# Performance work log

Hardware: AMD Instinct MI355X
Metric: run time of the kernel (lower is better)

## Reference

```python
import jax, jax.numpy as jnp
import numpy as np
from jax import lax

BETA = 0.9   # membrane decay
THR = 1.0    # firing threshold (soft reset)
K = 10       # number of time bins
# spatial pyramid for original_shape=(100,368) under 4 stride-2 SAME convs
HW = [(50, 184), (25, 92), (13, 46), (7, 23)]
CH = [4, 8, 16, 32]


def conv(x, w, b, stride=1):
    y = lax.conv_general_dilated(x, w, (stride, stride), 'SAME',
                                 dimension_numbers=('NCHW', 'OIHW', 'NCHW'))
    return y + b[None, :, None, None]


def spike(u):
    # heaviside forward, sigmoid straight-through surrogate backward
    s = (u > 0.0).astype(u.dtype)
    sg = jax.nn.sigmoid(4.0 * u)
    return sg + lax.stop_gradient(s - sg)


def setup_inputs() -> dict:
    key = jax.random.key(0)
    ks = jax.random.split(key, 12)
    T, B = 1000, 1
    x = jax.random.normal(ks[0], (T, B, 1, 100, 368), jnp.float32)

    def w(k, o, i, kh=3, kw=3):
        return 0.1 * jax.random.normal(k, (o, i, kh, kw), jnp.float32)

    inp = {'x': x}
    cin = [1] + CH[:3]
    for li in range(4):
        inp['w%d' % (li + 1)] = w(ks[1 + li], CH[li], cin[li])
        inp['b%d' % (li + 1)] = jnp.zeros((CH[li],), jnp.float32)
    sc = [2 * K * c for c in CH]  # skip channels: [80,160,320,640]
    inp['dw4'] = w(ks[5], 64, sc[3]); inp['db4'] = jnp.zeros((64,), jnp.float32)
    inp['dw3'] = w(ks[6], 32, 64 + sc[2]); inp['db3'] = jnp.zeros((32,), jnp.float32)
    inp['dw2'] = w(ks[7], 16, 32 + sc[1]); inp['db2'] = jnp.zeros((16,), jnp.float32)
    inp['dw1'] = w(ks[8], 8, 16 + sc[0]); inp['db1'] = jnp.zeros((8,), jnp.float32)
    inp['wo'] = w(ks[9], 1, 8, 1, 1); inp['bo'] = jnp.zeros((1,), jnp.float32)
    inp['total_steps'] = 1000
    inp['block_size'] = 100
    return inp


def reference(x, w1, b1, w2, b2, w3, b3, w4, b4,
              dw4, db4, dw3, db3, dw2, db2, dw1, db1, wo, bo,
              total_steps, block_size):
    S = total_steps // K  # steps per bin
    B = x.shape[1]
    xb = x.reshape((K, S) + x.shape[1:])  # [K,S,B,C,H,W]
    mems0 = tuple(jnp.zeros((B, CH[i], HW[i][0], HW[i][1]), x.dtype) for i in range(4))
    enc_w = [(w1, b1), (w2, b2), (w3, b3), (w4, b4)]

    def forward_step(x_t, mems):
        new_mems, spk = [], x_t
        for (wi, bi), m in zip(enc_w, mems):
            m = BETA * m + conv(spk, wi, bi, 2)
            spk = spike(m - THR)
            m = m - spk * THR  # soft reset
            new_mems.append(m)
        return tuple(new_mems)

    def step(carry, x_t):
        mems, sums, sqs = carry
        mems = forward_step(x_t, mems)
        sums = tuple(s + m for s, m in zip(sums, mems))
        sqs = tuple(q + m * m for q, m in zip(sqs, mems))
        return (mems, sums, sqs), None

    def bin_fn(mems, x_bin):
        zeros = tuple(jnp.zeros_like(m) for m in mems)
        (mems, sums, sqs), _ = lax.scan(step, (mems, zeros, zeros), x_bin)
        means = tuple(s / S for s in sums)
        stds = tuple(jnp.sqrt(jnp.maximum(q / S - mu * mu, 1e-8))
                     for q, mu in zip(sqs, means))
        return mems, (means, stds)

    _, (means, stds) = lax.scan(bin_fn, mems0, xb)  # each leaf: [K,B,C,H,W]

    def skip(mean, std):
        # torch.cat([mean0,std0,mean1,std1,...], dim=1) channel ordering
        f = jnp.stack([mean, std], axis=1)        # [K,2,B,C,H,W]
        f = jnp.transpose(f, (2, 0, 1, 3, 4, 5))  # [B,K,2,C,H,W]
        b_, k_, t_, c_, h_, w_ = f.shape
        return f.reshape(b_, k_ * t_ * c_, h_, w_)

    skips = [skip(means[i], stds[i]) for i in range(4)]

    def up(t, hw):
        return jax.image.resize(t, (t.shape[0], t.shape[1], hw[0], hw[1]), 'bilinear')

    relu = jax.nn.relu
    d = relu(conv(skips[3], dw4, db4))
    d = relu(conv(jnp.concatenate([up(d, HW[2]), skips[2]], 1), dw3, db3))
    d = relu(conv(jnp.concatenate([up(d, HW[1]), skips[1]], 1), dw2, db2))
    d = relu(conv(jnp.concatenate([up(d, HW[0]), skips[0]], 1), dw1, db1))
    tau_c = conv(up(d, (100, 368)), wo, bo)  # [B,1,100,368]
    return tau_c
```

## Files before the change

kernel.cpp:

```cpp
#include <hip/hip_runtime.h>

#define KBINS  10
#define SBIN   100
#define BETA   0.9f
#define THR    1.0f
#define CDIV(a,b) (((a)+(b)-1)/(b))


__global__ void k_row_zero(unsigned char* __restrict__ base, int planeStride,
                           int rowOff0, int rowOff1, int rowBytes, int nplanes) {
    int half = rowBytes >> 1;
    int per  = (rowOff1 >= 0 ? 2 : 1) * half;
    int n = blockIdx.x * blockDim.x + threadIdx.x;
    if (n >= nplanes * per) return;
    int pl = n / per;
    int r  = n - pl * per;
    int off = (r < half) ? (rowOff0 + 2 * r) : (rowOff1 + 2 * (r - half));
    *(unsigned short*)(base + (size_t)pl * planeStride + off) = 0;
}

__global__ void k_col_zero(unsigned char* __restrict__ base, int planeStride,
                           int Wp, int W, int H, int nplanes) {
    int n = blockIdx.x * blockDim.x + threadIdx.x;
    if (n >= nplanes * H) return;
    int pl = n / H;
    int r  = 1 + (n - pl * H);
    base[(size_t)pl * planeStride + r * Wp + (W + 1)] = 0;
}

__global__ void __launch_bounds__(256, 4)
k_conv1(const float* __restrict__ x,
        const float* __restrict__ w1,
        const float* __restrict__ b1,
        float* __restrict__ c1) {
    int n = blockIdx.x * blockDim.x + threadIdx.x;
    if (n >= 1000 * 50 * 23) return;
    int wq  = n % 23;
    int tmp = n / 23;
    int h   = tmp % 50;
    int t   = tmp / 50;
    int w0  = wq * 8;

    const float* xt = x + (size_t)t * 36800;
    float rm2 = (h < 49) ? 1.f : 0.f;
    int   r2  = min(2 * h + 2, 99);
    int   cb  = 2 * w0;
    float cm16 = (cb + 16 <= 367) ? 1.f : 0.f;
    int   c16  = min(cb + 16, 367);

    const float* row0 = xt + (2 * h) * 368 + cb;
    const float* row1 = row0 + 368;
    const float* row2 = xt + r2 * 368 + cb;

    float tap[3][17];
    {
        float4 a = *(const float4*)(row0);
        float4 b = *(const float4*)(row0 + 4);
        float4 c = *(const float4*)(row0 + 8);
        float4 d = *(const float4*)(row0 + 12);
        tap[0][0]=a.x;  tap[0][1]=a.y;  tap[0][2]=a.z;  tap[0][3]=a.w;
        tap[0][4]=b.x;  tap[0][5]=b.y;  tap[0][6]=b.z;  tap[0][7]=b.w;
        tap[0][8]=c.x;  tap[0][9]=c.y;  tap[0][10]=c.z; tap[0][11]=c.w;
        tap[0][12]=d.x; tap[0][13]=d.y; tap[0][14]=d.z; tap[0][15]=d.w;
    }
    {
        float4 a = *(const float4*)(row1);
        float4 b = *(const float4*)(row1 + 4);
        float4 c = *(const float4*)(row1 + 8);
        float4 d = *(const float4*)(row1 + 12);
        tap[1][0]=a.x;  tap[1][1]=a.y;  tap[1][2]=a.z;  tap[1][3]=a.w;
        tap[1][4]=b.x;  tap[1][5]=b.y;  tap[1][6]=b.z;  tap[1][7]=b.w;
        tap[1][8]=c.x;  tap[1][9]=c.y;  tap[1][10]=c.z; tap[1][11]=c.w;
        tap[1][12]=d.x; tap[1][13]=d.y; tap[1][14]=d.z; tap[1][15]=d.w;
    }
    {
        float4 a = *(const float4*)(row2);
        float4 b = *(const float4*)(row2 + 4);
        float4 c = *(const float4*)(row2 + 8);
        float4 d = *(const float4*)(row2 + 12);
        tap[2][0]=a.x*rm2;  tap[2][1]=a.y*rm2;  tap[2][2]=a.z*rm2;  tap[2][3]=a.w*rm2;
        tap[2][4]=b.x*rm2;  tap[2][5]=b.y*rm2;  tap[2][6]=b.z*rm2;  tap[2][7]=b.w*rm2;
        tap[2][8]=c.x*rm2;  tap[2][9]=c.y*rm2;  tap[2][10]=c.z*rm2; tap[2][11]=c.w*rm2;
        tap[2][12]=d.x*rm2; tap[2][13]=d.y*rm2; tap[2][14]=d.z*rm2; tap[2][15]=d.w*rm2;
    }
    tap[0][16] = xt[(2 * h) * 368 + c16] * cm16;
    tap[1][16] = xt[(2 * h + 1) * 368 + c16] * cm16;
    tap[2][16] = xt[r2 * 368 + c16] * (rm2 * cm16);

    float* ot = c1 + (size_t)t * 36800 + h * 184 + w0;
    #pragma unroll
    for (int co = 0; co < 4; co++) {
        float b = b1[co];
        float a[8];
        #pragma unroll
        for (int q = 0; q < 8; q++) a[q] = b;
        #pragma unroll
        for (int r = 0; r < 3; r++) {
            #pragma unroll
            for (int kw = 0; kw < 3; kw++) {
                float wv = w1[co * 9 + r * 3 + kw];
                #pragma unroll
                for (int q = 0; q < 8; q++)
                    a[q] = fmaf(tap[r][2 * q + kw], wv, a[q]);
            }
        }
        float* oc = ot + (size_t)co * 9200;
        *(float4*)(oc)     = make_float4(a[0], a[1], a[2], a[3]);
        *(float4*)(oc + 4) = make_float4(a[4], a[5], a[6], a[7]);
    }
}

__global__ void __launch_bounds__(64, 1)
k_scan(const float* __restrict__ cbuf,
       unsigned char* __restrict__ spk,
       float* __restrict__ skip,
       float* __restrict__ mscratch,
       int C, int HW, int Win, int Wp, int HpWp, int write_spk) {
    const int PF = 50;
    int CHW = C * HW;
    int p = blockIdx.x * blockDim.x + threadIdx.x;
    if (p >= CHW) return;
    int c  = p / HW;
    int hw = p - c * HW;
    int h  = hw / Win, w = hw - h * Win;

    const size_t tstr = (size_t)C * HpWp;
    unsigned char* sp = spk + (size_t)c * HpWp + (h + 1) * Wp + (w + 1);

    float m = 0.0f;
    float va[PF], vb[PF];
    #pragma unroll
    for (int j = 0; j < PF; j++) va[j] = cbuf[(size_t)j * CHW + p];

    for (int k = 0; k < KBINS; k++) {
        float s = 0.0f, q = 0.0f;

        {
            int tn = k * SBIN + PF;
            #pragma unroll
            for (int j = 0; j < PF; j++)
                vb[j] = cbuf[(size_t)(tn + j) * CHW + p];
            #pragma unroll
            for (int j = 0; j < PF; j++) {
                m = fmaf(m, BETA, va[j]);
                float spv = (m - THR > 0.0f) ? 1.0f : 0.0f;
                m -= spv * THR;
                if (write_spk) sp[(size_t)(k * SBIN + j) * tstr] = (unsigned char)spv;
                s += m;
                q = fmaf(m, m, q);
            }
        }
        {
            int tn = (k + 1) * SBIN;
            bool more = (k + 1 < KBINS);
            #pragma unroll
            for (int j = 0; j < PF; j++)
                va[j] = more ? cbuf[(size_t)(tn + j) * CHW + p] : 0.0f;
            #pragma unroll
            for (int j = 0; j < PF; j++) {
                m = fmaf(m, BETA, vb[j]);
                float spv = (m - THR > 0.0f) ? 1.0f : 0.0f;
                m -= spv * THR;
                if (write_spk) sp[(size_t)(k * SBIN + PF + j) * tstr] = (unsigned char)spv;
                s += m;
                q = fmaf(m, m, q);
            }
        }

        float mean = s * (1.0f / SBIN);
        float var  = q * (1.0f / SBIN) - mean * mean;
        float sd   = sqrtf(fmaxf(var, 1e-8f));
        skip[(size_t)(k * 2 * C + c) * HW + hw]     = mean;
        skip[(size_t)(k * 2 * C + C + c) * HW + hw] = sd;
    }
    mscratch[p] = m;
}

template<int CIN, int COUT, int COG, int OW,
         int HOUT, int WOUT, int PADH, int HP, int WP>
__global__ void k_convs2(const unsigned char* __restrict__ spk,
                         const float* __restrict__ wt,
                         const float* __restrict__ bias,
                         float* __restrict__ out) {
    const int WQ = (WOUT + OW - 1) / OW;
    const int NT = 2 * OW + 1;
    int n = blockIdx.x * blockDim.x + threadIdx.x;
    if (n >= 1000 * HOUT * WQ) return;
    int wq  = n % WQ;
    int tmp = n / WQ;
    int h   = tmp % HOUT;
    int t   = tmp / HOUT;
    int cog = blockIdx.y;
    int w0  = wq * OW;

    const unsigned char* base = spk + (size_t)t * CIN * HP * WP
                              + (2 * h - PADH + 1) * WP + (2 * w0 + 1);

    float acc[OW][COG];
    #pragma unroll
    for (int q = 0; q < OW; q++)
        #pragma unroll
        for (int co = 0; co < COG; co++) acc[q][co] = bias[cog * COG + co];

    for (int ci = 0; ci < CIN; ci++) {
        const unsigned char* ic = base + (size_t)ci * HP * WP;
        float tap[3][NT];
        #pragma unroll
        for (int r = 0; r < 3; r++)
            #pragma unroll
            for (int j = 0; j < NT; j++)
                tap[r][j] = (float)ic[r * WP + j];
        #pragma unroll
        for (int co = 0; co < COG; co++) {
            const float* wc = wt + ((size_t)(cog * COG + co) * CIN + ci) * 9;
            #pragma unroll
            for (int r = 0; r < 3; r++)
                #pragma unroll
                for (int kw = 0; kw < 3; kw++) {
                    float wv = wc[r * 3 + kw];
                    #pragma unroll
                    for (int q = 0; q < OW; q++)
                        acc[q][co] = fmaf(tap[r][2 * q + kw], wv, acc[q][co]);
                }
        }
    }

    float* ot = out + ((size_t)t * COUT + cog * COG) * (HOUT * WOUT) + h * WOUT + w0;
    #pragma unroll
    for (int co = 0; co < COG; co++) {
        float* oc = ot + (size_t)co * (HOUT * WOUT);
        if constexpr (OW == 4) {
            *(float4*)oc = make_float4(acc[0][co], acc[1][co], acc[2][co], acc[3][co]);
        } else {
            if (w0 + 2 <= WOUT) *(float2*)oc = make_float2(acc[0][co], acc[1][co]);
            else                oc[0] = acc[0][co];
        }
    }
}

__global__ void k_up_cat(const float* __restrict__ up_src, int Cup, int Hi, int Wi,
                         const float* __restrict__ skip, int Cskip,
                         float* __restrict__ out, int Ho, int Wo) {
    int total = (Cup + Cskip) * Ho * Wo;
    int n = blockIdx.x * blockDim.x + threadIdx.x;
    if (n >= total) return;
    int w   = n % Wo;
    int tmp = n / Wo;
    int h   = tmp % Ho;
    int c   = tmp / Ho;
    float v;
    if (c < Cup) {
        float ph = (h + 0.5f) * (float)Hi / (float)Ho - 0.5f;
        float pw = (w + 0.5f) * (float)Wi / (float)Wo - 0.5f;
        float fh = floorf(ph), fw = floorf(pw);
        int h0 = (int)fh, w0 = (int)fw;
        float ah = ph - fh, aw = pw - fw;
        int h0c = min(max(h0, 0), Hi - 1), h1c = min(max(h0 + 1, 0), Hi - 1);
        int w0c = min(max(w0, 0), Wi - 1), w1c = min(max(w0 + 1, 0), Wi - 1);
        const float* sc = up_src + (size_t)c * Hi * Wi;
        float v00 = sc[h0c * Wi + w0c], v01 = sc[h0c * Wi + w1c];
        float v10 = sc[h1c * Wi + w0c], v11 = sc[h1c * Wi + w1c];
        v = (1.0f - ah) * ((1.0f - aw) * v00 + aw * v01)
          + ah * ((1.0f - aw) * v10 + aw * v11);
    } else {
        v = skip[(size_t)(c - Cup) * Ho * Wo + h * Wo + w];
    }
    out[n] = v;
}

template<int CIN, int CS, int COG>
__global__ void k_dconv(const float* __restrict__ in,
                        const float* __restrict__ wt,
                        float* __restrict__ part,
                        int Cout, int H, int W) {
    int HW  = H * W;
    int pix = blockIdx.x * blockDim.x + threadIdx.x;
    if (pix >= HW) return;
    int co0   = blockIdx.y * COG;
    int chunk = blockIdx.z;
    int h = pix / W, w = pix - h * W;

    int off[9]; float msk[9];
    #pragma unroll
    for (int kh = 0; kh < 3; kh++) {
        int r = h + kh - 1;
        bool rok = (r >= 0) && (r < H);
        int rc = rok ? r : 0;
        #pragma unroll
        for (int kw = 0; kw < 3; kw++) {
            int cc = w + kw - 1;
            bool cok = (cc >= 0) && (cc < W);
            int ccc = cok ? cc : 0;
            off[kh * 3 + kw] = rc * W + ccc;
            msk[kh * 3 + kw] = (rok && cok) ? 1.0f : 0.0f;
        }
    }

    const float* ibase = in + (size_t)chunk * CS * HW;
    const float* wbase = wt + ((size_t)co0 * CIN + (size_t)chunk * CS) * 9;

    float acc[COG];
    #pragma unroll
    for (int co = 0; co < COG; co++) acc[co] = 0.0f;

    #pragma unroll 8
    for (int ci = 0; ci < CS; ci++) {
        const float* ic = ibase + (size_t)ci * HW;
        float tap[9];
        #pragma unroll
        for (int j = 0; j < 9; j++)
            tap[j] = msk[j] * ic[off[j]];
        #pragma unroll
        for (int co = 0; co < COG; co++) {
            const float* wc = wbase + ((size_t)co * CIN + ci) * 9;
            #pragma unroll
            for (int j = 0; j < 9; j++)
                acc[co] = fmaf(tap[j], wc[j], acc[co]);
        }
    }

    float* pp = part + ((size_t)chunk * Cout + co0) * HW + pix;
    #pragma unroll
    for (int co = 0; co < COG; co++) pp[(size_t)co * HW] = acc[co];
}

__global__ void k_reduce_relu(const float* __restrict__ part,
                              const float* __restrict__ bias,
                              float* __restrict__ out,
                              int Cout, int HW, int nchunks) {
    int n = blockIdx.x * blockDim.x + threadIdx.x;
    if (n >= Cout * HW) return;
    int co = n / HW;
    float acc = bias[co];
    for (int c = 0; c < nchunks; c++)
        acc += part[(size_t)c * Cout * HW + n];
    out[n] = fmaxf(acc, 0.0f);
}

__global__ void k_final(const float* __restrict__ d1,
                        const float* __restrict__ wo,
                        const float* __restrict__ bo,
                        float* __restrict__ out) {
    int n = blockIdx.x * blockDim.x + threadIdx.x;
    if (n >= 36800) return;
    int w = n % 368, h = n / 368;
    float ph = (h + 0.5f) * 0.5f - 0.5f;
    float pw = (w + 0.5f) * 0.5f - 0.5f;
    float fh = floorf(ph), fw = floorf(pw);
    int h0 = (int)fh, w0 = (int)fw;
    float ah = ph - fh, aw = pw - fw;
    int h0c = min(max(h0, 0), 49),  h1c = min(max(h0 + 1, 0), 49);
    int w0c = min(max(w0, 0), 183), w1c = min(max(w0 + 1, 0), 183);
    float acc = bo[0];
    #pragma unroll
    for (int c = 0; c < 8; c++) {
        const float* sc = d1 + c * 9200;
        float v00 = sc[h0c * 184 + w0c], v01 = sc[h0c * 184 + w1c];
        float v10 = sc[h1c * 184 + w0c], v11 = sc[h1c * 184 + w1c];
        float v = (1.0f - ah) * ((1.0f - aw) * v00 + aw * v01)
                + ah * ((1.0f - aw) * v10 + aw * v11);
        acc = fmaf(wo[c], v, acc);
    }
    out[n] = acc;
}

extern "C" void kernel_launch(void* const* d_in, const int* in_sizes, int n_in,
                              void* d_out, int out_size, void* d_ws, size_t ws_size,
                              hipStream_t stream) {
    (void)in_sizes; (void)n_in; (void)out_size; (void)ws_size;
    const float* x   = (const float*)d_in[0];
    const float* w1  = (const float*)d_in[1];
    const float* b1  = (const float*)d_in[2];
    const float* w2  = (const float*)d_in[3];
    const float* b2  = (const float*)d_in[4];
    const float* w3  = (const float*)d_in[5];
    const float* b3  = (const float*)d_in[6];
    const float* w4  = (const float*)d_in[7];
    const float* b4  = (const float*)d_in[8];
    const float* dw4 = (const float*)d_in[9];
    const float* db4 = (const float*)d_in[10];
    const float* dw3 = (const float*)d_in[11];
    const float* db3 = (const float*)d_in[12];
    const float* dw2 = (const float*)d_in[13];
    const float* db2 = (const float*)d_in[14];
    const float* dw1 = (const float*)d_in[15];
    const float* db1 = (const float*)d_in[16];
    const float* wo  = (const float*)d_in[17];
    const float* bo  = (const float*)d_in[18];
    float* out = (float*)d_out;

    char* ws = (char*)d_ws;
    size_t off = 0;
    auto alloc = [&](size_t bytes) -> void* {
        void* p = ws + off;
        off += (bytes + 255) & ~(size_t)255;
        return p;
    };
    float*         cbuf  = (float*)alloc(147200000);
    unsigned char* spk1p = (unsigned char*)alloc(39936000);
    unsigned char* spk2p = (unsigned char*)alloc(21600000);
    unsigned char* spk3p = (unsigned char*)alloc(12960000);
    float*         skip0 = (float*)alloc(2944000);
    float*         skip1 = (float*)alloc(1472000);
    float*         skip2 = (float*)alloc(765440);
    float*         skip3 = (float*)alloc(412160);
    float*         msS   = (float*)alloc(147200);
    char* dec = (char*)cbuf;
    size_t doff = 0;
    auto dalloc = [&](size_t bytes) -> void* {
        void* p = dec + doff;
        doff += (bytes + 255) & ~(size_t)255;
        return p;
    };
    float* d4   = (float*)dalloc(10304u * 4);
    float* d3   = (float*)dalloc(19136u * 4);
    float* d2   = (float*)dalloc(36800u * 4);
    float* d1   = (float*)dalloc(73600u * 4);
    float* cat3 = (float*)dalloc(229632u * 4);
    float* cat2 = (float*)dalloc(441600u * 4);
    float* cat1 = (float*)dalloc(883200u * 4);
    float* part = (float*)dalloc(230400u * 4);

    const int BS  = 256;
    const int SBS = 64;

    k_row_zero<<<CDIV(4000  *  96, BS), BS, 0, stream>>>(spk1p, 9984, 51 * 192, -1,   192, 4000);
    k_row_zero<<<CDIV(8000  * 100, BS), BS, 0, stream>>>(spk2p, 2700, 0,        2600, 100, 8000);
    k_row_zero<<<CDIV(16000 *  54, BS), BS, 0, stream>>>(spk3p,  810, 0,        756,  54,  16000);
    k_col_zero<<<CDIV(4000  *  50, BS), BS, 0, stream>>>(spk1p, 9984, 192, 184, 50, 4000);
    k_col_zero<<<CDIV(8000  *  25, BS), BS, 0, stream>>>(spk2p, 2700, 100,  92, 25, 8000);
    k_col_zero<<<CDIV(16000 *  13, BS), BS, 0, stream>>>(spk3p,  810,  54,  46, 13, 16000);

    k_conv1<<<CDIV(1000 * 50 * 23, BS), BS, 0, stream>>>(x, w1, b1, cbuf);
    k_scan<<<CDIV(36800, SBS), SBS, 0, stream>>>(cbuf, spk1p, skip0, msS,
                                                 4, 9200, 184, 192, 52 * 192, 1);

    k_convs2<4, 8, 8, 4, 25, 92, 0, 52, 192>
        <<<dim3(CDIV(1000 * 25 * 23, BS), 1), BS, 0, stream>>>(spk1p, w2, b2, cbuf);
    k_scan<<<CDIV(18400, SBS), SBS, 0, stream>>>(cbuf, spk2p, skip1, msS,
                                                 8, 2300, 92, 100, 27 * 100, 1);

    k_convs2<8, 16, 16, 2, 13, 46, 1, 27, 100>
        <<<dim3(CDIV(1000 * 13 * 23, BS), 1), BS, 0, stream>>>(spk2p, w3, b3, cbuf);
    k_scan<<<CDIV(9568, SBS), SBS, 0, stream>>>(cbuf, spk3p, skip2, msS,
                                                16, 598, 46, 54, 15 * 54, 1);

    k_convs2<16, 32, 16, 2, 7, 23, 1, 15, 54>
        <<<dim3(CDIV(1000 * 7 * 12, BS), 2), BS, 0, stream>>>(spk3p, w4, b4, cbuf);
    k_scan<<<CDIV(5152, SBS), SBS, 0, stream>>>(cbuf, spk1p , skip3, msS,
                                                32, 161, 23, 31, 9 * 31, 0);

    {
        dim3 g(CDIV(161, 64), 16, 20);
        k_dconv<640, 32, 4><<<g, 64, 0, stream>>>(skip3, dw4, part, 64, 7, 23);
        k_reduce_relu<<<CDIV(64 * 161, BS), BS, 0, stream>>>(part, db4, d4, 64, 161, 20);
    }
    {
        k_up_cat<<<CDIV(384 * 598, BS), BS, 0, stream>>>(d4, 64, 7, 23,
                                                         skip2, 320, cat3, 13, 46);
        dim3 g(CDIV(598, 64), 8, 12);
        k_dconv<384, 32, 4><<<g, 64, 0, stream>>>(cat3, dw3, part, 32, 13, 46);
        k_reduce_relu<<<CDIV(32 * 598, BS), BS, 0, stream>>>(part, db3, d3, 32, 598, 12);
    }
    {
        k_up_cat<<<CDIV(192 * 2300, BS), BS, 0, stream>>>(d3, 32, 13, 46,
                                                          skip1, 160, cat2, 25, 92);
        dim3 g(CDIV(2300, 128), 4, 6);
        k_dconv<192, 32, 4><<<g, 128, 0, stream>>>(cat2, dw2, part, 16, 25, 92);
        k_reduce_relu<<<CDIV(16 * 2300, BS), BS, 0, stream>>>(part, db2, d2, 16, 2300, 6);
    }
    {
        k_up_cat<<<CDIV(96 * 9200, BS), BS, 0, stream>>>(d2, 16, 25, 92,
                                                         skip0, 80, cat1, 50, 184);
        dim3 g(CDIV(9200, BS), 2, 3);
        k_dconv<96, 32, 4><<<g, BS, 0, stream>>>(cat1, dw1, part, 8, 50, 184);
        k_reduce_relu<<<CDIV(8 * 9200, BS), BS, 0, stream>>>(part, db1, d1, 8, 9200, 3);
    }
    k_final<<<CDIV(36800, BS), BS, 0, stream>>>(d1, wo, bo, out);
}
```

Before: 870.8 us.

## Fuse layer-1 convolution into the membrane scan kernel with register prefetch

Replaces the separate layer-1 conv kernel and its scan kernel with one kernel. Each thread computes its own 3x3 stride-2 conv tap straight from the input while it walks the time steps, and double-buffers five time steps of input in registers. This removes the write and re-read of the 147 MB layer-1 conv buffer. The cost is that every one of the four channels re-reads the same input pixels, with strided loads and only 36800 threads of 64-thread blocks, so occupancy and coalescing may suffer.

```diff
diff --git a/kernel.cpp b/kernel.cpp
--- a/kernel.cpp
+++ b/kernel.cpp
@@ -28,86 +28,91 @@
     base[(size_t)pl * planeStride + r * Wp + (W + 1)] = 0;
 }
 
-__global__ void __launch_bounds__(256, 4)
-k_conv1(const float* __restrict__ x,
-        const float* __restrict__ w1,
-        const float* __restrict__ b1,
-        float* __restrict__ c1) {
-    int n = blockIdx.x * blockDim.x + threadIdx.x;
-    if (n >= 1000 * 50 * 23) return;
-    int wq  = n % 23;
-    int tmp = n / 23;
-    int h   = tmp % 50;
-    int t   = tmp / 50;
-    int w0  = wq * 8;
-
-    const float* xt = x + (size_t)t * 36800;
-    float rm2 = (h < 49) ? 1.f : 0.f;
-    int   r2  = min(2 * h + 2, 99);
-    int   cb  = 2 * w0;
-    float cm16 = (cb + 16 <= 367) ? 1.f : 0.f;
-    int   c16  = min(cb + 16, 367);
-
-    const float* row0 = xt + (2 * h) * 368 + cb;
-    const float* row1 = row0 + 368;
-    const float* row2 = xt + r2 * 368 + cb;
-
-    float tap[3][17];
-    {
-        float4 a = *(const float4*)(row0);
-        float4 b = *(const float4*)(row0 + 4);
-        float4 c = *(const float4*)(row0 + 8);
-        float4 d = *(const float4*)(row0 + 12);
-        tap[0][0]=a.x;  tap[0][1]=a.y;  tap[0][2]=a.z;  tap[0][3]=a.w;
-        tap[0][4]=b.x;  tap[0][5]=b.y;  tap[0][6]=b.z;  tap[0][7]=b.w;
-        tap[0][8]=c.x;  tap[0][9]=c.y;  tap[0][10]=c.z; tap[0][11]=c.w;
-        tap[0][12]=d.x; tap[0][13]=d.y; tap[0][14]=d.z; tap[0][15]=d.w;
-    }
-    {
-        float4 a = *(const float4*)(row1);
-        float4 b = *(const float4*)(row1 + 4);
-        float4 c = *(const float4*)(row1 + 8);
-        float4 d = *(const float4*)(row1 + 12);
-        tap[1][0]=a.x;  tap[1][1]=a.y;  tap[1][2]=a.z;  tap[1][3]=a.w;
-        tap[1][4]=b.x;  tap[1][5]=b.y;  tap[1][6]=b.z;  tap[1][7]=b.w;
-        tap[1][8]=c.x;  tap[1][9]=c.y;  tap[1][10]=c.z; tap[1][11]=c.w;
-        tap[1][12]=d.x; tap[1][13]=d.y; tap[1][14]=d.z; tap[1][15]=d.w;
-    }
-    {
-        float4 a = *(const float4*)(row2);
-        float4 b = *(const float4*)(row2 + 4);
-        float4 c = *(const float4*)(row2 + 8);
-        float4 d = *(const float4*)(row2 + 12);
-        tap[2][0]=a.x*rm2;  tap[2][1]=a.y*rm2;  tap[2][2]=a.z*rm2;  tap[2][3]=a.w*rm2;
-        tap[2][4]=b.x*rm2;  tap[2][5]=b.y*rm2;  tap[2][6]=b.z*rm2;  tap[2][7]=b.w*rm2;
-        tap[2][8]=c.x*rm2;  tap[2][9]=c.y*rm2;  tap[2][10]=c.z*rm2; tap[2][11]=c.w*rm2;
-        tap[2][12]=d.x*rm2; tap[2][13]=d.y*rm2; tap[2][14]=d.z*rm2; tap[2][15]=d.w*rm2;
-    }
-    tap[0][16] = xt[(2 * h) * 368 + c16] * cm16;
-    tap[1][16] = xt[(2 * h + 1) * 368 + c16] * cm16;
-    tap[2][16] = xt[r2 * 368 + c16] * (rm2 * cm16);
-
-    float* ot = c1 + (size_t)t * 36800 + h * 184 + w0;
-    #pragma unroll
-    for (int co = 0; co < 4; co++) {
-        float b = b1[co];
-        float a[8];
-        #pragma unroll
-        for (int q = 0; q < 8; q++) a[q] = b;
-        #pragma unroll
-        for (int r = 0; r < 3; r++) {
-            #pragma unroll
-            for (int kw = 0; kw < 3; kw++) {
-                float wv = w1[co * 9 + r * 3 + kw];
-                #pragma unroll
-                for (int q = 0; q < 8; q++)
-                    a[q] = fmaf(tap[r][2 * q + kw], wv, a[q]);
-            }
-        }
-        float* oc = ot + (size_t)co * 9200;
-        *(float4*)(oc)     = make_float4(a[0], a[1], a[2], a[3]);
-        *(float4*)(oc + 4) = make_float4(a[4], a[5], a[6], a[7]);
-    }
+#define FS1_LOAD(DST, T0) do {                                                \
+    const float* xb_ = x + (size_t)(T0) * 36800;                              \
+    _Pragma("unroll")                                                         \
+    for (int j = 0; j < 5; j++) {                                             \
+        const float* xt_ = xb_ + j * 36800;                                   \
+        float2 v0_ = *(const float2*)(xt_ + ro0 + c0);                        \
+        float2 v1_ = *(const float2*)(xt_ + ro1 + c0);                        \
+        float2 v2_ = *(const float2*)(xt_ + ro2 + c0);                        \
+        DST[j][0] = v0_.x; DST[j][1] = v0_.y; DST[j][2] = xt_[ro0 + c2];      \
+        DST[j][3] = v1_.x; DST[j][4] = v1_.y; DST[j][5] = xt_[ro1 + c2];      \
+        DST[j][6] = v2_.x; DST[j][7] = v2_.y; DST[j][8] = xt_[ro2 + c2];      \
+    }                                                                         \
+} while (0)
+
+#define FS1_STEPS(SRC, T0) do {                                               \
+    _Pragma("unroll")                                                         \
+    for (int j = 0; j < 5; j++) {                                             \
+        float a_ = bb;                                                        \
+        a_ = fmaf(SRC[j][0],       wr0, a_);                                  \
+        a_ = fmaf(SRC[j][1],       wr1, a_);                                  \
+        a_ = fmaf(SRC[j][2] * cm,  wr2, a_);                                  \
+        a_ = fmaf(SRC[j][3],       wr3, a_);                                  \
+        a_ = fmaf(SRC[j][4],       wr4, a_);                                  \
+        a_ = fmaf(SRC[j][5] * cm,  wr5, a_);                                  \
+        a_ = fmaf(SRC[j][6] * rm2, wr6, a_);                                  \
+        a_ = fmaf(SRC[j][7] * rm2, wr7, a_);                                  \
+        a_ = fmaf(SRC[j][8] * rmcm, wr8, a_);                                 \
+        m = fmaf(m, BETA, a_);                                                \
+        float spv_ = (m - THR > 0.0f) ? 1.0f : 0.0f;                          \
+        m -= spv_ * THR;                                                      \
+        sp[(size_t)((T0) + j) * 39936] = (unsigned char)spv_;                 \
+        s += m;                                                               \
+        q = fmaf(m, m, q);                                                    \
+    }                                                                         \
+} while (0)
+
+__global__ void __launch_bounds__(64, 1)
+k_fscan1(const float* __restrict__ x,
+         const float* __restrict__ w1,
+         const float* __restrict__ b1,
+         unsigned char* __restrict__ spk,
+         float* __restrict__ skip,
+         float* __restrict__ mscratch) {
+    int p = blockIdx.x * blockDim.x + threadIdx.x;
+    if (p >= 36800) return;
+    int c  = p / 9200;
+    int hw = p - c * 9200;
+    int h  = hw / 184, w = hw - h * 184;
+
+    float rm2  = (h < 49) ? 1.f : 0.f;
+    float cm   = (2 * w + 2 <= 367) ? 1.f : 0.f;
+    float rmcm = rm2 * cm;
+    int ro0 = (2 * h) * 368;
+    int ro1 = ro0 + 368;
+    int ro2 = min(2 * h + 2, 99) * 368;
+    int c0  = 2 * w;
+    int c2  = min(2 * w + 2, 367);
+
+    float wr0 = w1[c * 9 + 0], wr1 = w1[c * 9 + 1], wr2 = w1[c * 9 + 2];
+    float wr3 = w1[c * 9 + 3], wr4 = w1[c * 9 + 4], wr5 = w1[c * 9 + 5];
+    float wr6 = w1[c * 9 + 6], wr7 = w1[c * 9 + 7], wr8 = w1[c * 9 + 8];
+    float bb  = b1[c];
+
+    unsigned char* sp = spk + (size_t)c * 9984 + (h + 1) * 192 + (w + 1);
+
+    float m = 0.0f;
+    float A[5][9], B[5][9];
+    FS1_LOAD(A, 0);
+
+    for (int k = 0; k < KBINS; k++) {
+        float s = 0.0f, q = 0.0f;
+        for (int gp = 0; gp < 10; gp++) {
+            int tA = k * SBIN + gp * 10;
+            FS1_LOAD(B, tA + 5);
+            FS1_STEPS(A, tA);
+            if (tA + 10 < 1000) FS1_LOAD(A, tA + 10);
+            FS1_STEPS(B, tA + 5);
+        }
+        float mean = s * (1.0f / SBIN);
+        float var  = q * (1.0f / SBIN) - mean * mean;
+        float sd   = sqrtf(fmaxf(var, 1e-8f));
+        skip[(size_t)(k * 8 + c) * 9200 + hw]       = mean;
+        skip[(size_t)(k * 8 + 4 + c) * 9200 + hw]   = sd;
+    }
+    mscratch[p] = m;
 }
 
 __global__ void __launch_bounds__(64, 1)
@@ -431,9 +436,7 @@
     k_col_zero<<<CDIV(8000  *  25, BS), BS, 0, stream>>>(spk2p, 2700, 100,  92, 25, 8000);
     k_col_zero<<<CDIV(16000 *  13, BS), BS, 0, stream>>>(spk3p,  810,  54,  46, 13, 16000);
 
-    k_conv1<<<CDIV(1000 * 50 * 23, BS), BS, 0, stream>>>(x, w1, b1, cbuf);
-    k_scan<<<CDIV(36800, SBS), SBS, 0, stream>>>(cbuf, spk1p, skip0, msS,
-                                                 4, 9200, 184, 192, 52 * 192, 1);
+    k_fscan1<<<CDIV(36800, SBS), SBS, 0, stream>>>(x, w1, b1, spk1p, skip0, msS);
 
     k_convs2<4, 8, 8, 4, 25, 92, 0, 52, 192>
         <<<dim3(CDIV(1000 * 25 * 23, BS), 1), BS, 0, stream>>>(spk1p, w2, b2, cbuf);
```

Result: slower. 955.3 us (+9.7%).
